# Optimization experiments

Hardware: AMD Instinct MI355X
Metric: run time of the kernel (lower is better)

Reference implementation:

```python
import jax, jax.numpy as jnp
import numpy as np

HID = 256
POS_FREQ = 10
DIR_FREQ = 4
POS_ENC = 3 * (2 * POS_FREQ + 1)   # 63
DIR_ENC = 3 * (2 * DIR_FREQ + 1)   # 27
N_PTS = 262144


def _posenc(x, num_freq):
    freqs = (2.0 ** jnp.arange(num_freq)).astype(x.dtype)      # [F]
    xf = x[..., None, :] * freqs[:, None]                       # [..., F, D]
    sc = jnp.stack([jnp.sin(xf), jnp.cos(xf)], axis=-2)         # [..., F, 2, D]
    return jnp.concatenate([x, sc.reshape(*x.shape[:-1], -1)], axis=-1)


def _linear_init(key, fan_in, fan_out):
    kw, kb = jax.random.split(key)
    s = 1.0 / np.sqrt(fan_in)
    W = jax.random.uniform(kw, (fan_in, fan_out), jnp.float32, -s, s)
    b = jax.random.uniform(kb, (fan_out,), jnp.float32, -s, s)
    return W, b


def setup_inputs() -> dict:
    key = jax.random.key(0)
    ks = jax.random.split(key, 16)
    inp = {
        "positions": jax.random.normal(ks[0], (N_PTS, 3), jnp.float32),
        "directions": jax.random.normal(ks[1], (N_PTS, 3), jnp.float32),
    }
    W, b = _linear_init(ks[2], POS_ENC, HID)
    inp["W_in"], inp["b_in"] = W, b
    # 7 hidden layers; layer index 4 takes skip concat (HID + POS_ENC)
    for i in range(7):
        fan_in = HID + POS_ENC if i == 4 else HID
        W, b = _linear_init(ks[3 + i], fan_in, HID)
        inp[f"W_h{i}"], inp[f"b_h{i}"] = W, b
    W, b = _linear_init(ks[10], HID, HID + 1)
    inp["W_out"], inp["b_out"] = W, b
    W, b = _linear_init(ks[11], HID + DIR_ENC, HID // 2)
    inp["W_r1"], inp["b_r1"] = W, b
    W, b = _linear_init(ks[12], HID // 2, 3)
    inp["W_r2"], inp["b_r2"] = W, b
    return inp


def _forward(positions, directions, W_in, b_in, hidden_params, W_out, b_out,
             W_r1, b_r1, W_r2, b_r2):
    pe = _posenc(positions, POS_FREQ)    # [N, 63]
    de = _posenc(directions, DIR_FREQ)   # [N, 27]
    h = jax.nn.relu(pe @ W_in + b_in)    # [N, 256]
    for i, (W, b) in enumerate(hidden_params):
        if i == 4:
            h = jnp.concatenate([h, pe], axis=-1)  # skip connection [N, 319]
        h = jax.nn.relu(h @ W + b)
    out = h @ W_out + b_out                      # [N, 257]
    features = out[..., :HID]                    # [N, 256]
    density = jax.nn.relu(out[..., HID:HID + 1])  # [N, 1]
    rgb_in = jnp.concatenate([features, de], axis=-1)  # [N, 283]
    rgb = jax.nn.sigmoid(jax.nn.relu(rgb_in @ W_r1 + b_r1) @ W_r2 + b_r2)  # [N, 3]
    return rgb, density


def reference(positions, directions, W_in, b_in,
              W_h0, b_h0, W_h1, b_h1, W_h2, b_h2, W_h3, b_h3,
              W_h4, b_h4, W_h5, b_h5, W_h6, b_h6,
              W_out, b_out, W_r1, b_r1, W_r2, b_r2):
    hidden = [(W_h0, b_h0), (W_h1, b_h1), (W_h2, b_h2), (W_h3, b_h3),
              (W_h4, b_h4), (W_h5, b_h5), (W_h6, b_h6)]
    return _forward(positions, directions, W_in, b_in, hidden,
                    W_out, b_out, W_r1, b_r1, W_r2, b_r2)
```

## Files before the change

kernel.cpp:

```cpp
#include <hip/hip_runtime.h>
#include <math.h>

#define NPTS 262144
#define MT 64

typedef __attribute__((ext_vector_type(8))) short bf16x8;
typedef __attribute__((ext_vector_type(4))) float f32x4;
typedef __attribute__((ext_vector_type(16))) float f32x16;
typedef __attribute__((ext_vector_type(2))) unsigned int u32x2;

#if defined(__has_builtin)
#if __has_builtin(__builtin_amdgcn_cvt_pk_bf16_f32)
#define HAVE_CVT_PK_BF16 1
#endif
#endif

__device__ __forceinline__ short f2bf(float f) {
    union { float f; unsigned u; } v; v.f = f;
    unsigned r = v.u + 0x7fffu + ((v.u >> 16) & 1u);
    return (short)(r >> 16);
}
__device__ __forceinline__ unsigned pk2(float a, float b) {
#ifdef HAVE_CVT_PK_BF16
    auto r = __builtin_amdgcn_cvt_pk_bf16_f32(a, b);
    unsigned u; __builtin_memcpy(&u, &r, 4);
    return u;
#else
    return ((unsigned)(unsigned short)f2bf(a)) |
           ((unsigned)(unsigned short)f2bf(b) << 16);
#endif
}

#define OFF_IN   0
#define SZ_IN    (64*256)
#define OFF_H0   (OFF_IN + SZ_IN)
#define SZ_H     (256*256)
#define OFF_H1   (OFF_H0 + SZ_H)
#define OFF_H2   (OFF_H1 + SZ_H)
#define OFF_H3   (OFF_H2 + SZ_H)
#define OFF_H4   (OFF_H3 + SZ_H)
#define SZ_H4    (320*256)
#define OFF_H5   (OFF_H4 + SZ_H4)
#define OFF_H6   (OFF_H5 + SZ_H)
#define OFF_OUT  (OFF_H6 + SZ_H)
#define SZ_OUTM  (256*256)
#define OFF_OUTD (OFF_OUT + SZ_OUTM)
#define SZ_OUTD  (256*16)
#define OFF_R1   (OFF_OUTD + SZ_OUTD)
#define SZ_R1    (288*128)
#define OFF_R2   (OFF_R1 + SZ_R1)
#define SZ_R2    (128*16)
#define WS_TOTAL (OFF_R2 + SZ_R2)

struct PrepP { const float* W[11]; short* ws; };

__global__ __launch_bounds__(256) void prep_all(PrepP pp) {
    int i = blockIdx.x * 256 + threadIdx.x;
    if (i >= WS_TOTAL) return;
    const int offs[13] = {OFF_IN, OFF_H0, OFF_H1, OFF_H2, OFF_H3, OFF_H4,
                          OFF_H5, OFF_H6, OFF_OUT, OFF_OUTD, OFF_R1, OFF_R2,
                          WS_TOTAL};
    const int wsrc[12] = {0,1,2,3,4,5,6,7,8,8,9,10};
    const int Ks[12]   = {63,256,256,256,256,319,256,256,256,256,283,128};
    const int Nsrc[12] = {256,256,256,256,256,256,256,256,257,257,128,3};
    int seg = 0;
    while (i >= offs[seg + 1]) seg++;
    int li = i - offs[seg];
    int j = li & 7, L = (li >> 3) & 63, tile = li >> 9;
    const float* W = pp.W[wsrc[seg]];
    float v = 0.f;
    if (seg == 9) {
        int k = tile * 32 + ((L >> 4) << 3) + j;
        if (k < 256 && (L & 15) == 0) v = W[k * 257 + 256];
    } else if (seg == 11) {
        int k = tile * 32 + ((L >> 4) << 3) + j;
        int n = L & 15;
        if (k < 128 && n < 3) v = W[k * 3 + n];
    } else {
        int nNb = (seg == 10) ? 4 : 8;
        int nb = tile % nNb, kt = tile / nNb;
        int k = kt * 16 + ((L >> 5) << 3) + j;
        int n = nb * 32 + (L & 31);
        if (k < Ks[seg]) v = W[k * Nsrc[seg] + n];
    }
    pp.ws[i] = f2bf(v);
}

struct Params {
    const float *pos, *dir;
    const float *b_in, *b_h0, *b_h1, *b_h2, *b_h3, *b_h4, *b_h5, *b_h6;
    const float *b_out, *b_r1, *b_r2;
    const short *w;
    float *out;
};

template<int NKT, int NNB, int TM, int MODE>
__device__ __forceinline__ void layer32(const short* __restrict__ Wsw,
                                        const short* __restrict__ Wd,
                                        const float* __restrict__ bias,
                                        const short* Xin, short* Xout,
                                        float* dout, int p0,
                                        int nb, int mbB, int wave, int lane) {
    const int l31 = lane & 31, hi = lane >> 5;
    const short* xb = Xin + hi * 512 + l31 * 8 + mbB * 256;
    const short* wp = Wsw + (size_t)(nb * 64 + lane) * 8;

    bf16x8 a0 = *(const bf16x8*)(wp);
    bf16x8 a1 = *(const bf16x8*)(wp + (size_t)NNB * 512);

    __syncthreads();

    if (MODE == 1 && wave < 4) {
        const int l15 = lane & 15, quad = lane >> 4;
        const short* xd = Xin + quad * 512 + (wave * 16 + l15) * 8;
        f32x4 ad = (f32x4){0.f, 0.f, 0.f, 0.f};
#pragma unroll
        for (int kt = 0; kt < 8; ++kt) {
            bf16x8 b = *(const bf16x8*)(xd + kt * 2048);
            bf16x8 a = *(const bf16x8*)(Wd + (size_t)(kt * 64 + lane) * 8);
            ad = __builtin_amdgcn_mfma_f32_16x16x32_bf16(a, b, ad, 0, 0, 0);
        }
        if (quad == 0)
            dout[3 * NPTS + p0 + wave * 16 + l15] = fmaxf(ad[0] + bias[256], 0.f);
    }

    f32x16 acc[TM];
#pragma unroll
    for (int t = 0; t < TM; t++)
#pragma unroll
        for (int r = 0; r < 16; r++) acc[t][r] = 0.f;

    bf16x8 b_c[TM];
#pragma unroll
    for (int t = 0; t < TM; t++)
        b_c[t] = *(const bf16x8*)(xb + t * 256);

#pragma unroll
    for (int kt = 0; kt < NKT; ++kt) {
        bf16x8 b_n[TM], a_n;
        if (kt + 1 < NKT) {
#pragma unroll
            for (int t = 0; t < TM; t++)
                b_n[t] = *(const bf16x8*)(xb + (kt + 1) * 1024 + t * 256);
        }
        if (kt + 2 < NKT)
            a_n = *(const bf16x8*)(wp + (size_t)(kt + 2) * NNB * 512);
        if ((kt & 1) == 0) {
#pragma unroll
            for (int t = 0; t < TM; t++)
                acc[t] = __builtin_amdgcn_mfma_f32_32x32x16_bf16(a0, b_c[t], acc[t], 0, 0, 0);
        } else {
#pragma unroll
            for (int t = 0; t < TM; t++)
                acc[t] = __builtin_amdgcn_mfma_f32_32x32x16_bf16(a1, b_c[t], acc[t], 0, 0, 0);
        }
        if (kt + 2 < NKT) {
            if ((kt & 1) == 0) a0 = a_n; else a1 = a_n;
        }
        if (kt + 1 < NKT) {
#pragma unroll
            for (int t = 0; t < TM; t++) b_c[t] = b_n[t];
        }
    }

#pragma unroll
    for (int t = 0; t < TM; t++) {
        const int m = (mbB + t) * 32 + l31;
#pragma unroll
        for (int rq = 0; rq < 4; rq++) {
            const int nbase = nb * 32 + rq * 8 + hi * 4;
            const f32x4 bv = *(const f32x4*)(bias + nbase);
            float v0 = acc[t][rq * 4 + 0] + bv[0];
            float v1 = acc[t][rq * 4 + 1] + bv[1];
            float v2 = acc[t][rq * 4 + 2] + bv[2];
            float v3 = acc[t][rq * 4 + 3] + bv[3];
            if (MODE == 0) {
                v0 = fmaxf(v0, 0.f); v1 = fmaxf(v1, 0.f);
                v2 = fmaxf(v2, 0.f); v3 = fmaxf(v3, 0.f);
            }
            u32x2 w; w[0] = pk2(v0, v1); w[1] = pk2(v2, v3);
            *(u32x2*)(Xout + ((size_t)(nb * 4 + rq) * 64 + m) * 8 + hi * 4) = w;
        }
    }
}

__global__ __launch_bounds__(512, 4) void nerf_fused(Params P) {
    __shared__ __align__(16) short XA[32 * 512];
    __shared__ __align__(16) short XB[40 * 512];
    const int tid = threadIdx.x;
    const int wave = tid >> 6, lane = tid & 63;
    const int p0 = blockIdx.x * MT;

    {
        const int pt = tid & 63, g = tid >> 6;
        const float x0 = P.pos[(p0 + pt) * 3 + 0];
        const float x1 = P.pos[(p0 + pt) * 3 + 1];
        const float x2 = P.pos[(p0 + pt) * 3 + 2];
        bf16x8 v;
#pragma unroll
        for (int j = 0; j < 8; j++) {
            const int d = g * 8 + j;
            float val = 0.f;
            if (d < 3) val = (d == 0) ? x0 : (d == 1) ? x1 : x2;
            else if (d < 63) {
                const int e = d - 3, f = e / 6, r = e % 6;
                const float x = (r % 3 == 0) ? x0 : (r % 3 == 1) ? x1 : x2;
                const float xf = x * (float)(1 << f);
                val = (r < 3) ? sinf(xf) : cosf(xf);
            }
            v[j] = f2bf(val);
        }
        *(bf16x8*)(XA + ((size_t)g * 64 + pt) * 8) = v;
        *(bf16x8*)(XB + ((size_t)(32 + g) * 64 + pt) * 8) = v;
    }

    bf16x8 de_v;
    if (wave < 4) {
        const int pt = tid & 63, g = wave;
        const float x0 = P.dir[(p0 + pt) * 3 + 0];
        const float x1 = P.dir[(p0 + pt) * 3 + 1];
        const float x2 = P.dir[(p0 + pt) * 3 + 2];
#pragma unroll
        for (int j = 0; j < 8; j++) {
            const int d = g * 8 + j;
            float val = 0.f;
            if (d < 3) val = (d == 0) ? x0 : (d == 1) ? x1 : x2;
            else if (d < 27) {
                const int e = d - 3, f = e / 6, r = e % 6;
                const float x = (r % 3 == 0) ? x0 : (r % 3 == 1) ? x1 : x2;
                const float xf = x * (float)(1 << f);
                val = (r < 3) ? sinf(xf) : cosf(xf);
            }
            de_v[j] = f2bf(val);
        }
    }

    layer32< 4, 8, 2, 0>(P.w + OFF_IN, nullptr, P.b_in, XA, XB, P.out, p0, wave, 0, wave, lane);
    layer32<16, 8, 2, 0>(P.w + OFF_H0, nullptr, P.b_h0, XB, XA, P.out, p0, wave, 0, wave, lane);
    layer32<16, 8, 2, 0>(P.w + OFF_H1, nullptr, P.b_h1, XA, XB, P.out, p0, wave, 0, wave, lane);
    layer32<16, 8, 2, 0>(P.w + OFF_H2, nullptr, P.b_h2, XB, XA, P.out, p0, wave, 0, wave, lane);
    layer32<16, 8, 2, 0>(P.w + OFF_H3, nullptr, P.b_h3, XA, XB, P.out, p0, wave, 0, wave, lane);
    layer32<20, 8, 2, 0>(P.w + OFF_H4, nullptr, P.b_h4, XB, XA, P.out, p0, wave, 0, wave, lane);
    layer32<16, 8, 2, 0>(P.w + OFF_H5, nullptr, P.b_h5, XA, XB, P.out, p0, wave, 0, wave, lane);

    if (wave < 4)
        *(bf16x8*)(XB + ((size_t)(32 + wave) * 64 + (tid & 63)) * 8) = de_v;

    layer32<16, 8, 2, 0>(P.w + OFF_H6, nullptr, P.b_h6, XB, XA, P.out, p0, wave, 0, wave, lane);
    layer32<16, 8, 2, 1>(P.w + OFF_OUT, P.w + OFF_OUTD, P.b_out, XA, XB, P.out, p0, wave, 0, wave, lane);

    layer32<18, 4, 1, 0>(P.w + OFF_R1, nullptr, P.b_r1, XB, XA, P.out, p0, wave & 3, wave >> 2, wave, lane);

    __syncthreads();
    if (wave < 4) {
        const int l15 = lane & 15, quad = lane >> 4;
        f32x4 acc = (f32x4){0.f, 0.f, 0.f, 0.f};
        const short* xb = XA + quad * 512 + (wave * 16 + l15) * 8;
#pragma unroll
        for (int kt = 0; kt < 4; ++kt) {
            bf16x8 b = *(const bf16x8*)(xb + kt * 2048);
            bf16x8 a = *(const bf16x8*)(P.w + OFF_R2 + (size_t)(kt * 64 + lane) * 8);
            acc = __builtin_amdgcn_mfma_f32_16x16x32_bf16(a, b, acc, 0, 0, 0);
        }
        if (quad == 0) {
#pragma unroll
            for (int r = 0; r < 3; r++) {
                const float v = acc[r] + P.b_r2[r];
                P.out[(size_t)(p0 + wave * 16 + l15) * 3 + r] = 1.f / (1.f + expf(-v));
            }
        }
    }
}

extern "C" void kernel_launch(void* const* d_in, const int* in_sizes, int n_in,
                              void* d_out, int out_size, void* d_ws, size_t ws_size,
                              hipStream_t stream) {
    short* ws = (short*)d_ws;

    PrepP pp;
    pp.W[0]  = (const float*)d_in[2];
    pp.W[1]  = (const float*)d_in[4];
    pp.W[2]  = (const float*)d_in[6];
    pp.W[3]  = (const float*)d_in[8];
    pp.W[4]  = (const float*)d_in[10];
    pp.W[5]  = (const float*)d_in[12];
    pp.W[6]  = (const float*)d_in[14];
    pp.W[7]  = (const float*)d_in[16];
    pp.W[8]  = (const float*)d_in[18];
    pp.W[9]  = (const float*)d_in[20];
    pp.W[10] = (const float*)d_in[22];
    pp.ws = ws;
    hipLaunchKernelGGL(prep_all, dim3((WS_TOTAL + 255) / 256), dim3(256), 0, stream, pp);

    Params P;
    P.pos  = (const float*)d_in[0];
    P.dir  = (const float*)d_in[1];
    P.b_in = (const float*)d_in[3];
    P.b_h0 = (const float*)d_in[5];
    P.b_h1 = (const float*)d_in[7];
    P.b_h2 = (const float*)d_in[9];
    P.b_h3 = (const float*)d_in[11];
    P.b_h4 = (const float*)d_in[13];
    P.b_h5 = (const float*)d_in[15];
    P.b_h6 = (const float*)d_in[17];
    P.b_out = (const float*)d_in[19];
    P.b_r1 = (const float*)d_in[21];
    P.b_r2 = (const float*)d_in[23];
    P.w = ws;
    P.out = (float*)d_out;
    hipLaunchKernelGGL(nerf_fused, dim3(NPTS / MT), dim3(512), 0, stream, P);
}
```

Baseline: 437.9 us.

## Double point tile to 128 and use single in-place LDS activation buffer

Raises points per block from 64 to 128, so each wave computes four 32-row M tiles per layer and each loaded weight fragment is reused across twice as many points. The ping-pong XA/XB buffers become one 80KB LDS buffer updated in place, with an extra barrier between the MMA loop and the write-back to keep it safe. The density and final RGB stages now run on all 8 waves instead of 4. The cost is double the accumulator registers and larger LDS per block, which can lower occupancy below the 4 blocks per CU requested by the launch bounds.

```diff
diff --git a/kernel.cpp b/kernel.cpp
--- a/kernel.cpp
+++ b/kernel.cpp
@@ -2,7 +2,7 @@
 #include <math.h>
 
 #define NPTS 262144
-#define MT 64
+#define MT 128
 
 typedef __attribute__((ext_vector_type(8))) short bf16x8;
 typedef __attribute__((ext_vector_type(4))) float f32x4;
@@ -98,11 +98,10 @@
 __device__ __forceinline__ void layer32(const short* __restrict__ Wsw,
                                         const short* __restrict__ Wd,
                                         const float* __restrict__ bias,
-                                        const short* Xin, short* Xout,
-                                        float* dout, int p0,
+                                        short* X, float* dout, int p0,
                                         int nb, int mbB, int wave, int lane) {
     const int l31 = lane & 31, hi = lane >> 5;
-    const short* xb = Xin + hi * 512 + l31 * 8 + mbB * 256;
+    const short* xb = X + hi * 1024 + (mbB * 32 + l31) * 8;
     const short* wp = Wsw + (size_t)(nb * 64 + lane) * 8;
 
     bf16x8 a0 = *(const bf16x8*)(wp);
@@ -110,13 +109,13 @@
 
     __syncthreads();
 
-    if (MODE == 1 && wave < 4) {
+    if (MODE == 1) {
         const int l15 = lane & 15, quad = lane >> 4;
-        const short* xd = Xin + quad * 512 + (wave * 16 + l15) * 8;
+        const short* xd = X + quad * 1024 + (wave * 16 + l15) * 8;
         f32x4 ad = (f32x4){0.f, 0.f, 0.f, 0.f};
 #pragma unroll
         for (int kt = 0; kt < 8; ++kt) {
-            bf16x8 b = *(const bf16x8*)(xd + kt * 2048);
+            bf16x8 b = *(const bf16x8*)(xd + kt * 4096);
             bf16x8 a = *(const bf16x8*)(Wd + (size_t)(kt * 64 + lane) * 8);
             ad = __builtin_amdgcn_mfma_f32_16x16x32_bf16(a, b, ad, 0, 0, 0);
         }
@@ -141,7 +140,7 @@
         if (kt + 1 < NKT) {
 #pragma unroll
             for (int t = 0; t < TM; t++)
-                b_n[t] = *(const bf16x8*)(xb + (kt + 1) * 1024 + t * 256);
+                b_n[t] = *(const bf16x8*)(xb + (kt + 1) * 2048 + t * 256);
         }
         if (kt + 2 < NKT)
             a_n = *(const bf16x8*)(wp + (size_t)(kt + 2) * NNB * 512);
@@ -162,6 +161,8 @@
             for (int t = 0; t < TM; t++) b_c[t] = b_n[t];
         }
     }
+
+    __syncthreads();
 
 #pragma unroll
     for (int t = 0; t < TM; t++) {
@@ -179,20 +180,19 @@
                 v2 = fmaxf(v2, 0.f); v3 = fmaxf(v3, 0.f);
             }
             u32x2 w; w[0] = pk2(v0, v1); w[1] = pk2(v2, v3);
-            *(u32x2*)(Xout + ((size_t)(nb * 4 + rq) * 64 + m) * 8 + hi * 4) = w;
+            *(u32x2*)(X + (size_t)(nb * 4 + rq) * 1024 + m * 8 + hi * 4) = w;
         }
     }
 }
 
 __global__ __launch_bounds__(512, 4) void nerf_fused(Params P) {
-    __shared__ __align__(16) short XA[32 * 512];
-    __shared__ __align__(16) short XB[40 * 512];
+    __shared__ __align__(16) short X[40 * 1024];
     const int tid = threadIdx.x;
     const int wave = tid >> 6, lane = tid & 63;
     const int p0 = blockIdx.x * MT;
 
-    {
-        const int pt = tid & 63, g = tid >> 6;
+    for (int i = tid; i < 128 * 8; i += 512) {
+        const int pt = i & 127, g = i >> 7;
         const float x0 = P.pos[(p0 + pt) * 3 + 0];
         const float x1 = P.pos[(p0 + pt) * 3 + 1];
         const float x2 = P.pos[(p0 + pt) * 3 + 2];
@@ -210,19 +210,19 @@
             }
             v[j] = f2bf(val);
         }
-        *(bf16x8*)(XA + ((size_t)g * 64 + pt) * 8) = v;
-        *(bf16x8*)(XB + ((size_t)(32 + g) * 64 + pt) * 8) = v;
+        *(bf16x8*)(X + ((size_t)g * 128 + pt) * 8) = v;
+        *(bf16x8*)(X + ((size_t)(32 + g) * 128 + pt) * 8) = v;
     }
 
     bf16x8 de_v;
-    if (wave < 4) {
-        const int pt = tid & 63, g = wave;
-        const float x0 = P.dir[(p0 + pt) * 3 + 0];
-        const float x1 = P.dir[(p0 + pt) * 3 + 1];
-        const float x2 = P.dir[(p0 + pt) * 3 + 2];
+    const int ptD = tid & 127, gD = tid >> 7;
+    {
+        const float x0 = P.dir[(p0 + ptD) * 3 + 0];
+        const float x1 = P.dir[(p0 + ptD) * 3 + 1];
+        const float x2 = P.dir[(p0 + ptD) * 3 + 2];
 #pragma unroll
         for (int j = 0; j < 8; j++) {
-            const int d = g * 8 + j;
+            const int d = gD * 8 + j;
             float val = 0.f;
             if (d < 3) val = (d == 0) ? x0 : (d == 1) ? x1 : x2;
             else if (d < 27) {
@@ -235,30 +235,29 @@
         }
     }
 
-    layer32< 4, 8, 2, 0>(P.w + OFF_IN, nullptr, P.b_in, XA, XB, P.out, p0, wave, 0, wave, lane);
-    layer32<16, 8, 2, 0>(P.w + OFF_H0, nullptr, P.b_h0, XB, XA, P.out, p0, wave, 0, wave, lane);
-    layer32<16, 8, 2, 0>(P.w + OFF_H1, nullptr, P.b_h1, XA, XB, P.out, p0, wave, 0, wave, lane);
-    layer32<16, 8, 2, 0>(P.w + OFF_H2, nullptr, P.b_h2, XB, XA, P.out, p0, wave, 0, wave, lane);
-    layer32<16, 8, 2, 0>(P.w + OFF_H3, nullptr, P.b_h3, XA, XB, P.out, p0, wave, 0, wave, lane);
-    layer32<20, 8, 2, 0>(P.w + OFF_H4, nullptr, P.b_h4, XB, XA, P.out, p0, wave, 0, wave, lane);
-    layer32<16, 8, 2, 0>(P.w + OFF_H5, nullptr, P.b_h5, XA, XB, P.out, p0, wave, 0, wave, lane);
-
-    if (wave < 4)
-        *(bf16x8*)(XB + ((size_t)(32 + wave) * 64 + (tid & 63)) * 8) = de_v;
-
-    layer32<16, 8, 2, 0>(P.w + OFF_H6, nullptr, P.b_h6, XB, XA, P.out, p0, wave, 0, wave, lane);
-    layer32<16, 8, 2, 1>(P.w + OFF_OUT, P.w + OFF_OUTD, P.b_out, XA, XB, P.out, p0, wave, 0, wave, lane);
-
-    layer32<18, 4, 1, 0>(P.w + OFF_R1, nullptr, P.b_r1, XB, XA, P.out, p0, wave & 3, wave >> 2, wave, lane);
+    layer32< 4, 8, 4, 0>(P.w + OFF_IN, nullptr, P.b_in, X, P.out, p0, wave, 0, wave, lane);
+    layer32<16, 8, 4, 0>(P.w + OFF_H0, nullptr, P.b_h0, X, P.out, p0, wave, 0, wave, lane);
+    layer32<16, 8, 4, 0>(P.w + OFF_H1, nullptr, P.b_h1, X, P.out, p0, wave, 0, wave, lane);
+    layer32<16, 8, 4, 0>(P.w + OFF_H2, nullptr, P.b_h2, X, P.out, p0, wave, 0, wave, lane);
+    layer32<16, 8, 4, 0>(P.w + OFF_H3, nullptr, P.b_h3, X, P.out, p0, wave, 0, wave, lane);
+    layer32<20, 8, 4, 0>(P.w + OFF_H4, nullptr, P.b_h4, X, P.out, p0, wave, 0, wave, lane);
+
+    *(bf16x8*)(X + ((size_t)(32 + gD) * 128 + ptD) * 8) = de_v;
+
+    layer32<16, 8, 4, 0>(P.w + OFF_H5, nullptr, P.b_h5, X, P.out, p0, wave, 0, wave, lane);
+    layer32<16, 8, 4, 0>(P.w + OFF_H6, nullptr, P.b_h6, X, P.out, p0, wave, 0, wave, lane);
+    layer32<16, 8, 4, 1>(P.w + OFF_OUT, P.w + OFF_OUTD, P.b_out, X, P.out, p0, wave, 0, wave, lane);
+
+    layer32<18, 4, 2, 0>(P.w + OFF_R1, nullptr, P.b_r1, X, P.out, p0, wave & 3, (wave >> 2) * 2, wave, lane);
 
     __syncthreads();
-    if (wave < 4) {
+    {
         const int l15 = lane & 15, quad = lane >> 4;
         f32x4 acc = (f32x4){0.f, 0.f, 0.f, 0.f};
-        const short* xb = XA + quad * 512 + (wave * 16 + l15) * 8;
+        const short* xb = X + quad * 1024 + (wave * 16 + l15) * 8;
 #pragma unroll
         for (int kt = 0; kt < 4; ++kt) {
-            bf16x8 b = *(const bf16x8*)(xb + kt * 2048);
+            bf16x8 b = *(const bf16x8*)(xb + kt * 4096);
             bf16x8 a = *(const bf16x8*)(P.w + OFF_R2 + (size_t)(kt * 64 + lane) * 8);
             acc = __builtin_amdgcn_mfma_f32_16x16x32_bf16(a, b, acc, 0, 0, 0);
         }
```

New measurement: 402.6 us. 8.0% less time.
